# Kernel tuning notes

Measured on AMD Instinct MI355X. Metric: run time of the kernel, lower is better.

The kernel has to match this reference:

```python
import jax, jax.numpy as jnp
import numpy as np

A = 9          # num anchors (RPN.anchor_list)
H = W = 32     # feature-map spatial size (scaled-up from 7x7)
HID = 256      # ProposalModule hidden dim
THRESH = 0.5       # inference() thresh default
NMS_THRESH = 0.7   # inference() nms_thresh default
N = H * W * A


def _conv(x, w, b):
    y = jax.lax.conv_general_dilated(x, w, (1, 1), 'SAME',
                                     dimension_numbers=('NCHW', 'OIHW', 'NCHW'))
    return y + b[None, :, None, None]


def _pairwise_iou(boxes):
    # boxes: (N,4) [x1,y1,x2,y2]
    x1, y1, x2, y2 = boxes[:, 0], boxes[:, 1], boxes[:, 2], boxes[:, 3]
    area = jnp.maximum(x2 - x1, 0.) * jnp.maximum(y2 - y1, 0.)
    iw = jnp.maximum(jnp.minimum(x2[:, None], x2[None, :]) - jnp.maximum(x1[:, None], x1[None, :]), 0.)
    ih = jnp.maximum(jnp.minimum(y2[:, None], y2[None, :]) - jnp.maximum(y1[:, None], y1[None, :]), 0.)
    inter = iw * ih
    return inter / (area[:, None] + area[None, :] - inter + 1e-8)


def _nms_keep(boxes, scores, valid, iou_thresh):
    # greedy NMS over ALL boxes; invalid (below conf-thresh) boxes start suppressed
    n = boxes.shape[0]
    order = jnp.argsort(-scores)
    b = boxes[order]
    v = valid[order]
    iou = _pairwise_iou(b)            # (N,N) -- dominant memory traffic
    idx = jnp.arange(n)

    def body(i, sup):
        alive = jnp.logical_not(sup[i])
        return sup | (alive & (iou[i] > iou_thresh) & (idx > i))

    sup = jax.lax.fori_loop(0, n, body, jnp.logical_not(v))
    return jnp.zeros(n, bool).at[order].set(jnp.logical_not(sup))


def setup_inputs() -> dict:
    key = jax.random.key(0)
    ks = jax.random.split(key, 4)
    feat = jax.random.normal(ks[0], (1, 1280, H, W), jnp.float32)
    anchors_wh = jnp.array([[1, 1], [2, 2], [3, 3], [4, 4], [5, 5],
                            [2, 3], [3, 2], [3, 5], [5, 3]], jnp.float32)
    w1 = jax.random.normal(ks[1], (HID, 1280, 3, 3), jnp.float32) * 0.01
    b1 = jnp.zeros((HID,), jnp.float32)
    w2 = jax.random.normal(ks[2], (6 * A, HID, 1, 1), jnp.float32) * 0.05
    b2 = jax.random.normal(ks[3], (6 * A,), jnp.float32) * 0.05
    return {"feat": feat, "anchors_wh": anchors_wh, "w1": w1, "b1": b1, "w2": w2, "b2": b2}


def reference(feat, anchors_wh, w1, b1, w2, b2):
    # ProposalModule: 3x3 conv + LeakyReLU + 1x1 conv to 6A channels (dropout is identity at inference)
    h = jax.nn.leaky_relu(_conv(feat, w1, b1), 0.01)
    out = _conv(h, w2, b2)[0].reshape(A, 6, H, W)   # batch 1 -> (A,6,H,W)
    conf = jax.nn.sigmoid(out[:, 0])                 # (A,H,W), sigmoid(conf_scores[:,0])
    offs = out[:, 2:6].transpose(0, 2, 3, 1)         # (A,H,W,4) = offsets.permute(0,2,3,1)

    # GenerateGrid: cell centers at +0.5; GenerateAnchor: wh-sized boxes on each center
    xs = jnp.arange(W, dtype=feat.dtype) + 0.5
    ys = jnp.arange(H, dtype=feat.dtype) + 0.5
    cx = xs[None, None, :]
    cy = ys[None, :, None]
    aw = anchors_wh[:, 0][:, None, None]
    ah = anchors_wh[:, 1][:, None, None]

    tx, ty, tw, th = offs[..., 0], offs[..., 1], offs[..., 2], offs[..., 3]
    pcx = cx + tx * aw
    pcy = cy + ty * ah
    pw = aw * jnp.exp(tw)
    ph = ah * jnp.exp(th)
    boxes = jnp.stack([pcx - pw / 2, pcy - ph / 2, pcx + pw / 2, pcy + ph / 2], -1)  # (A,H,W,4)

    conf_f = conf.transpose(1, 2, 0).reshape(-1)          # (H*W*A,) = permute(1,2,0).reshape(-1)
    boxes_f = boxes.transpose(1, 2, 0, 3).reshape(-1, 4)  # (H*W*A,4)

    valid = conf_f > THRESH
    scores = jnp.where(valid, conf_f, -1.0)
    keep = _nms_keep(boxes_f, scores, valid, NMS_THRESH)

    k = keep.astype(boxes_f.dtype)[:, None]
    # fixed-shape masked output: kept rows are [x1,y1,x2,y2,conf], suppressed rows are 0
    return jnp.concatenate([boxes_f * k, conf_f[:, None] * k], axis=-1)  # (N,5)
```

## Files before the change

kernel.cpp:

```cpp
#include <hip/hip_runtime.h>
#include <math.h>

#define NPIX 1024
#define NBOX 9216
#define ECAP 6144

typedef unsigned long long u64;

#define O_PART     0u
#define O_H        0u
#define O_BOXES    1048576u
#define O_CONF     1196032u
#define O_KEYS     1232896u
#define O_ORDER    1306624u
#define O_SBOX     1343488u
#define O_SAREA    1490944u
#define O_EDGES    1527808u
#define O_KEEPW    1552384u
#define O_RPART    1553920u
#define O_VCNT     16777216u
#define O_ECNT     16777220u


__global__ __launch_bounds__(256, 4) void conv1_kernel(const float* __restrict__ feat,
                                                       const float* __restrict__ w1,
                                                       float* __restrict__ partial,
                                                       int* __restrict__ VE) {
    const int kc  = blockIdx.x;
    const int cog = blockIdx.y;
    const int tid = threadIdx.x;
    const int x0 = (tid & 7) * 4;
    const int y  = tid >> 3;
    const int ci0 = kc * 80;
    const int co0 = cog * 4;

    if (kc == 0 && cog == 0 && tid < 2) VE[tid] = 0;

    __shared__ float sf[8 * 34 * 32];

    for (int e = tid; e < 8 * 2 * 32; e += 256) {
        int ci_l = e >> 6, r = (e >> 5) & 1, c = e & 31;
        sf[(ci_l * 34 + r * 33) * 32 + c] = 0.f;
    }

    float acc[4][4];
#pragma unroll
    for (int a = 0; a < 4; ++a)
#pragma unroll
        for (int b = 0; b < 4; ++b) acc[a][b] = 0.f;

    const float* wbase = w1 + (size_t)co0 * 11520 + (size_t)ci0 * 9;

    for (int chunk = 0; chunk < 10; ++chunk) {
        const int cbase = ci0 + chunk * 8;
        __syncthreads();
        {
            const float4* fg = (const float4*)(feat + (size_t)cbase * NPIX);
#pragma unroll
            for (int k = 0; k < 8; ++k) {
                int e = tid + k * 256;
                int ci_l = e >> 8, rem = e & 255;
                int row = rem >> 3, f4c = rem & 7;
                float4 v = fg[ci_l * 256 + rem];
                *(float4*)&sf[(ci_l * 34 + row + 1) * 32 + f4c * 4] = v;
            }
        }
        __syncthreads();

#pragma unroll
        for (int cil = 0; cil < 8; ++cil) {
            float f[3][6];
            const float* base = &sf[(cil * 34 + y) * 32];
#pragma unroll
            for (int dy = 0; dy < 3; ++dy) {
                const float* rp = base + dy * 32;
                float4 mid = *(const float4*)(rp + x0);
                float lft = __int_as_float(__builtin_amdgcn_update_dpp(
                    0, __float_as_int(mid.w), 0x111 , 0xF, 0xF, true));
                float rgt = __int_as_float(__builtin_amdgcn_update_dpp(
                    0, __float_as_int(mid.x), 0x101 , 0xF, 0xF, true));
                f[dy][0] = (x0 == 0) ? 0.f : lft;
                f[dy][1] = mid.x; f[dy][2] = mid.y; f[dy][3] = mid.z; f[dy][4] = mid.w;
                f[dy][5] = (x0 == 28) ? 0.f : rgt;
            }
#pragma unroll
            for (int co = 0; co < 4; ++co) {
                const float* wrow = wbase + (size_t)co * 11520 +
                                    (size_t)(chunk * 8 + cil) * 9;
                float wv[9];
#pragma unroll
                for (int t = 0; t < 9; ++t) wv[t] = wrow[t];
#pragma unroll
                for (int dy = 0; dy < 3; ++dy)
#pragma unroll
                    for (int dx = 0; dx < 3; ++dx) {
                        float wgt = wv[dy * 3 + dx];
#pragma unroll
                        for (int px = 0; px < 4; ++px)
                            acc[co][px] = fmaf(f[dy][px + dx], wgt, acc[co][px]);
                    }
            }
        }
    }

    const int pix = y * 32 + x0;
#pragma unroll
    for (int co = 0; co < 4; ++co) {
        float4 v = {acc[co][0], acc[co][1], acc[co][2], acc[co][3]};
        *(float4*)&partial[((size_t)kc * 256 + co0 + co) * NPIX + pix] = v;
    }
}

__global__ __launch_bounds__(256) void conv1_reduce(float* part_h,
                                                    const float* __restrict__ b1) {
    int i = blockIdx.x * 256 + threadIdx.x;
    float s = b1[i >> 10];
#pragma unroll
    for (int kc = 0; kc < 16; ++kc) s += part_h[(size_t)kc * 262144 + i];
    part_h[i] = s > 0.f ? s : 0.01f * s;
}

__global__ __launch_bounds__(256) void conv2_decode(const float* __restrict__ h,
                                                    const float* __restrict__ w2,
                                                    const float* __restrict__ b2,
                                                    const float* __restrict__ anchors,
                                                    float* __restrict__ boxes,
                                                    float* __restrict__ conf_arr,
                                                    u64* __restrict__ keys,
                                                    int* __restrict__ Vcnt) {
    int gid = blockIdx.x * 256 + threadIdx.x;
    int box = gid >> 3, q = gid & 7;
    int a = box >> 10, p = box & 1023;
    const float* hq  = h + (size_t)(q * 32) * NPIX + p;
    const float* wq  = w2 + (size_t)(a * 6) * 256 + q * 32;
    float s0 = 0.f, s2 = 0.f, s3 = 0.f, s4 = 0.f, s5 = 0.f;
#pragma unroll 4
    for (int ci = 0; ci < 32; ++ci) {
        float hv = hq[(size_t)ci * NPIX];
        s0 = fmaf(hv, wq[0 * 256 + ci], s0);
        s2 = fmaf(hv, wq[2 * 256 + ci], s2);
        s3 = fmaf(hv, wq[3 * 256 + ci], s3);
        s4 = fmaf(hv, wq[4 * 256 + ci], s4);
        s5 = fmaf(hv, wq[5 * 256 + ci], s5);
    }
    s0 += __shfl_xor(s0, 1); s0 += __shfl_xor(s0, 2); s0 += __shfl_xor(s0, 4);
    s2 += __shfl_xor(s2, 1); s2 += __shfl_xor(s2, 2); s2 += __shfl_xor(s2, 4);
    s3 += __shfl_xor(s3, 1); s3 += __shfl_xor(s3, 2); s3 += __shfl_xor(s3, 4);
    s4 += __shfl_xor(s4, 1); s4 += __shfl_xor(s4, 2); s4 += __shfl_xor(s4, 4);
    s5 += __shfl_xor(s5, 1); s5 += __shfl_xor(s5, 2); s5 += __shfl_xor(s5, 4);
    if (q == 0) {
        s0 += b2[a * 6 + 0];
        s2 += b2[a * 6 + 2];
        s3 += b2[a * 6 + 3];
        s4 += b2[a * 6 + 4];
        s5 += b2[a * 6 + 5];
        float conf = 1.f / (1.f + expf(-s0));
        float x = (float)(p & 31), yy = (float)(p >> 5);
        float cx = x + 0.5f, cy = yy + 0.5f;
        float aw = anchors[a * 2 + 0], ah = anchors[a * 2 + 1];
        float pcx = cx + s2 * aw, pcy = cy + s3 * ah;
        float pw = aw * expf(s4), ph = ah * expf(s5);
        int idx = p * 9 + a;
        boxes[idx * 4 + 0] = pcx - pw / 2.f;
        boxes[idx * 4 + 1] = pcy - ph / 2.f;
        boxes[idx * 4 + 2] = pcx + pw / 2.f;
        boxes[idx * 4 + 3] = pcy + ph / 2.f;
        conf_arr[idx] = conf;
        bool valid = conf > 0.5f;
        float score = valid ? conf : -1.0f;
        unsigned int sb = __float_as_uint(score);
        sb = (sb & 0x80000000u) ? ~sb : (sb | 0x80000000u);
        keys[idx] = ((u64)sb << 32) | (unsigned int)(~idx);
        if (valid) atomicAdd(Vcnt, 1);
    }
}

__global__ __launch_bounds__(256) void rank_partial(const u64* __restrict__ keys,
                                                    int* __restrict__ rpart) {
    __shared__ u64 sk[256];
    int i = blockIdx.x * 256 + threadIdx.x;
    sk[threadIdx.x] = keys[blockIdx.y * 256 + threadIdx.x];
    __syncthreads();
    u64 ki = keys[i];
    int c = 0;
#pragma unroll 8
    for (int j = 0; j < 256; ++j) c += (sk[j] > ki) ? 1 : 0;
    rpart[blockIdx.y * NBOX + i] = c;
}

__global__ __launch_bounds__(256) void rank_reduce_gather(const int* __restrict__ rpart,
                                                          const float* __restrict__ boxes,
                                                          int* __restrict__ order,
                                                          float* __restrict__ sbox,
                                                          float* __restrict__ sarea) {
    int i = blockIdx.x * 256 + threadIdx.x;
    int r = 0;
    for (int b = 0; b < 36; ++b) r += rpart[b * NBOX + i];
    order[r] = i;
    float x1 = boxes[i * 4 + 0], y1 = boxes[i * 4 + 1];
    float x2 = boxes[i * 4 + 2], y2 = boxes[i * 4 + 3];
    sbox[r * 4 + 0] = x1; sbox[r * 4 + 1] = y1;
    sbox[r * 4 + 2] = x2; sbox[r * 4 + 3] = y2;
    sarea[r] = fmaxf(x2 - x1, 0.f) * fmaxf(y2 - y1, 0.f);
}

__global__ __launch_bounds__(256) void nms_edges(const float* __restrict__ sbox,
                                                 const float* __restrict__ sarea,
                                                 const int* __restrict__ Vp,
                                                 unsigned* __restrict__ edges,
                                                 int* __restrict__ Ecnt) {
    int V = *Vp;
    int lane = threadIdx.x & 63;
    for (int i = blockIdx.x; i < V; i += 2048) {
        float x1i = sbox[i * 4 + 0], y1i = sbox[i * 4 + 1];
        float x2i = sbox[i * 4 + 2], y2i = sbox[i * 4 + 3];
        float ai = sarea[i];
        for (int j = i + 1 + threadIdx.x; ; j += 256) {
            bool active = (j < V);
            if (__ballot(active) == 0ull) break;
            bool hit = false;
            if (active) {
                float x1j = sbox[j * 4 + 0], y1j = sbox[j * 4 + 1];
                float x2j = sbox[j * 4 + 2], y2j = sbox[j * 4 + 3];
                float iw = fmaxf(fminf(x2i, x2j) - fmaxf(x1i, x1j), 0.f);
                float ih = fmaxf(fminf(y2i, y2j) - fmaxf(y1i, y1j), 0.f);
                float inter = iw * ih;
                float iou = inter / (ai + sarea[j] - inter + 1e-8f);
                hit = iou > 0.7f;
            }
            u64 bal = __ballot(hit);
            if (bal) {
                int cnt = __popcll(bal);
                unsigned base = 0;
                if (lane == 0) base = (unsigned)atomicAdd(Ecnt, cnt);
                base = (unsigned)__shfl((int)base, 0, 64);
                if (hit) {
                    int pos = (int)base + __popcll(bal & ((1ull << lane) - 1ull));
                    if (pos < ECAP) edges[pos] = ((unsigned)j << 16) | (unsigned)i;
                }
            }
        }
    }
}

__global__ __launch_bounds__(256) void nms_resolve(const unsigned* __restrict__ edges,
                                                   const int* __restrict__ Ep,
                                                   const int* __restrict__ Vp,
                                                   u64* __restrict__ keepw) {
    __shared__ unsigned se[ECAP];
    __shared__ unsigned ss[ECAP];
    __shared__ u64 sup[144];
    const int tid = threadIdx.x;
    int E = *Ep; if (E > ECAP) E = ECAP;
    const int V = *Vp;
    for (int e = tid; e < E; e += 256) se[e] = edges[e];
    for (int w = tid; w < 144; w += 256) sup[w] = 0;
    __syncthreads();
    for (int e = tid; e < E; e += 256) {
        unsigned k = se[e];
        int r = 0;
        for (int q = 0; q < E; ++q) r += (se[q] < k) ? 1 : 0;
        ss[r] = k;
    }
    __syncthreads();
    if (tid == 0) {
        for (int e = 0; e < E; ++e) {
            unsigned k = ss[e];
            int i = (int)(k & 0xffffu), j = (int)(k >> 16);
            if (!((sup[i >> 6] >> (i & 63)) & 1ull))
                sup[j >> 6] |= 1ull << (j & 63);
        }
    }
    __syncthreads();
    for (int w = tid; w < 144; w += 256) {
        int base = w * 64;
        u64 vm;
        if (base + 64 <= V) vm = ~0ull;
        else if (base >= V) vm = 0ull;
        else vm = (1ull << (V - base)) - 1ull;
        keepw[w] = ~sup[w] & vm;
    }
}

__global__ __launch_bounds__(256) void finalize(const int* __restrict__ order,
                                                const int* __restrict__ Vp,
                                                const u64* __restrict__ keepw,
                                                const float* __restrict__ boxes,
                                                const float* __restrict__ conf_arr,
                                                float* __restrict__ out) {
    int p = blockIdx.x * 256 + threadIdx.x;
    int V = *Vp;
    int o = order[p];
    bool keep = false;
    if (p < V) keep = (keepw[p >> 6] >> (p & 63)) & 1ull;
    float k = keep ? 1.f : 0.f;
    out[o * 5 + 0] = boxes[o * 4 + 0] * k;
    out[o * 5 + 1] = boxes[o * 4 + 1] * k;
    out[o * 5 + 2] = boxes[o * 4 + 2] * k;
    out[o * 5 + 3] = boxes[o * 4 + 3] * k;
    out[o * 5 + 4] = conf_arr[o] * k;
}

extern "C" void kernel_launch(void* const* d_in, const int* in_sizes, int n_in,
                              void* d_out, int out_size, void* d_ws, size_t ws_size,
                              hipStream_t stream) {
    const float* feat    = (const float*)d_in[0];
    const float* anchors = (const float*)d_in[1];
    const float* w1      = (const float*)d_in[2];
    const float* b1      = (const float*)d_in[3];
    const float* w2      = (const float*)d_in[4];
    const float* b2      = (const float*)d_in[5];
    float* out = (float*)d_out;

    char* ws = (char*)d_ws;
    float* partial = (float*)(ws + O_PART);
    float* h       = (float*)(ws + O_H);
    float* boxes   = (float*)(ws + O_BOXES);
    float* conf    = (float*)(ws + O_CONF);
    u64*   keys    = (u64*)(ws + O_KEYS);
    int* rpart     = (int*)(ws + O_RPART);
    int* order     = (int*)(ws + O_ORDER);
    float* sbox    = (float*)(ws + O_SBOX);
    float* sarea   = (float*)(ws + O_SAREA);
    int* Vcnt      = (int*)(ws + O_VCNT);
    int* Ecnt      = (int*)(ws + O_ECNT);
    u64* keepw     = (u64*)(ws + O_KEEPW);
    unsigned* edges = (unsigned*)(ws + O_EDGES);

    conv1_kernel<<<dim3(16, 64), 256, 0, stream>>>(feat, w1, partial, Vcnt);
    conv1_reduce<<<1024, 256, 0, stream>>>(partial, b1);
    conv2_decode<<<288, 256, 0, stream>>>(h, w2, b2, anchors, boxes, conf, keys, Vcnt);
    rank_partial<<<dim3(36, 36), 256, 0, stream>>>(keys, rpart);
    rank_reduce_gather<<<36, 256, 0, stream>>>(rpart, boxes, order, sbox, sarea);
    nms_edges<<<2048, 256, 0, stream>>>(sbox, sarea, Vcnt, edges, Ecnt);
    nms_resolve<<<1, 256, 0, stream>>>(edges, Ecnt, Vcnt, keepw);
    finalize<<<36, 256, 0, stream>>>(order, Vcnt, keepw, boxes, conf, out);
}
```

Baseline: 226.1 us.

## Fuse post-conv pipeline stages into one cooperative persistent kernel with grid syncs

Replaces the seven kernels after conv1 (reduce, conv2/decode, rank, gather, NMS edges, resolve, finalize) with a single cooperative kernel of 512 blocks separated by grid.sync barriers. It falls back to the original launch sequence if the cooperative launch fails. The aim is to remove per-kernel launch gaps and tail effects in the small latency-bound stages. In exchange, each stage runs on a fixed 512-block grid instead of its own launch shape, the big shared arrays limit occupancy, and grid-wide barriers have their own cost.

```diff
diff --git a/kernel.cpp b/kernel.cpp
--- a/kernel.cpp
+++ b/kernel.cpp
@@ -1,9 +1,13 @@
 #include <hip/hip_runtime.h>
+#include <hip/hip_cooperative_groups.h>
 #include <math.h>
+
+namespace cg = cooperative_groups;
 
 #define NPIX 1024
 #define NBOX 9216
 #define ECAP 6144
+#define TGRID 512
 
 typedef unsigned long long u64;
 
@@ -301,6 +305,202 @@
     out[o * 5 + 4] = conf_arr[o] * k;
 }
 
+__global__ __launch_bounds__(256, 2) void tail_mega(float* part_h,
+                                                    const float* __restrict__ b1,
+                                                    const float* __restrict__ w2,
+                                                    const float* __restrict__ b2,
+                                                    const float* __restrict__ anchors,
+                                                    float* __restrict__ boxes,
+                                                    float* __restrict__ conf_arr,
+                                                    u64* __restrict__ keys,
+                                                    int* __restrict__ Vcnt,
+                                                    int* __restrict__ Ecnt,
+                                                    int* __restrict__ rpart,
+                                                    int* __restrict__ order,
+                                                    float* __restrict__ sbox,
+                                                    float* __restrict__ sarea,
+                                                    unsigned* __restrict__ edges,
+                                                    u64* __restrict__ keepw,
+                                                    float* __restrict__ out) {
+    cg::grid_group grid = cg::this_grid();
+    const int tid = threadIdx.x;
+    const int bid = blockIdx.x;
+
+    __shared__ u64 sk[256];
+    __shared__ unsigned se[ECAP];
+    __shared__ unsigned ss[ECAP];
+    __shared__ u64 sup[144];
+
+    for (int i = bid * 256 + tid; i < 262144; i += TGRID * 256) {
+        float s = b1[i >> 10];
+#pragma unroll
+        for (int kc = 0; kc < 16; ++kc) s += part_h[(size_t)kc * 262144 + i];
+        part_h[i] = s > 0.f ? s : 0.01f * s;
+    }
+    grid.sync();
+
+    for (int vb = bid; vb < 288; vb += TGRID) {
+        int gid = vb * 256 + tid;
+        int box = gid >> 3, q = gid & 7;
+        int a = box >> 10, p = box & 1023;
+        const float* hq  = part_h + (size_t)(q * 32) * NPIX + p;
+        const float* wq  = w2 + (size_t)(a * 6) * 256 + q * 32;
+        float s0 = 0.f, s2 = 0.f, s3 = 0.f, s4 = 0.f, s5 = 0.f;
+#pragma unroll 4
+        for (int ci = 0; ci < 32; ++ci) {
+            float hv = hq[(size_t)ci * NPIX];
+            s0 = fmaf(hv, wq[0 * 256 + ci], s0);
+            s2 = fmaf(hv, wq[2 * 256 + ci], s2);
+            s3 = fmaf(hv, wq[3 * 256 + ci], s3);
+            s4 = fmaf(hv, wq[4 * 256 + ci], s4);
+            s5 = fmaf(hv, wq[5 * 256 + ci], s5);
+        }
+        s0 += __shfl_xor(s0, 1); s0 += __shfl_xor(s0, 2); s0 += __shfl_xor(s0, 4);
+        s2 += __shfl_xor(s2, 1); s2 += __shfl_xor(s2, 2); s2 += __shfl_xor(s2, 4);
+        s3 += __shfl_xor(s3, 1); s3 += __shfl_xor(s3, 2); s3 += __shfl_xor(s3, 4);
+        s4 += __shfl_xor(s4, 1); s4 += __shfl_xor(s4, 2); s4 += __shfl_xor(s4, 4);
+        s5 += __shfl_xor(s5, 1); s5 += __shfl_xor(s5, 2); s5 += __shfl_xor(s5, 4);
+        if (q == 0) {
+            s0 += b2[a * 6 + 0];
+            s2 += b2[a * 6 + 2];
+            s3 += b2[a * 6 + 3];
+            s4 += b2[a * 6 + 4];
+            s5 += b2[a * 6 + 5];
+            float conf = 1.f / (1.f + expf(-s0));
+            float x = (float)(p & 31), yy = (float)(p >> 5);
+            float cx = x + 0.5f, cy = yy + 0.5f;
+            float aw = anchors[a * 2 + 0], ah = anchors[a * 2 + 1];
+            float pcx = cx + s2 * aw, pcy = cy + s3 * ah;
+            float pw = aw * expf(s4), ph = ah * expf(s5);
+            int idx = p * 9 + a;
+            boxes[idx * 4 + 0] = pcx - pw / 2.f;
+            boxes[idx * 4 + 1] = pcy - ph / 2.f;
+            boxes[idx * 4 + 2] = pcx + pw / 2.f;
+            boxes[idx * 4 + 3] = pcy + ph / 2.f;
+            conf_arr[idx] = conf;
+            bool valid = conf > 0.5f;
+            float score = valid ? conf : -1.0f;
+            unsigned int sb = __float_as_uint(score);
+            sb = (sb & 0x80000000u) ? ~sb : (sb | 0x80000000u);
+            keys[idx] = ((u64)sb << 32) | (unsigned int)(~idx);
+            if (valid) atomicAdd(Vcnt, 1);
+        }
+    }
+    grid.sync();
+
+    for (int v = bid; v < 1296; v += TGRID) {
+        int bx = v % 36, by = v / 36;
+        sk[tid] = keys[by * 256 + tid];
+        __syncthreads();
+        int i = bx * 256 + tid;
+        u64 ki = keys[i];
+        int c = 0;
+#pragma unroll 8
+        for (int j = 0; j < 256; ++j) c += (sk[j] > ki) ? 1 : 0;
+        rpart[by * NBOX + i] = c;
+        __syncthreads();
+    }
+    grid.sync();
+
+    for (int v = bid; v < 36; v += TGRID) {
+        int i = v * 256 + tid;
+        int r = 0;
+        for (int b = 0; b < 36; ++b) r += rpart[b * NBOX + i];
+        order[r] = i;
+        float x1 = boxes[i * 4 + 0], y1 = boxes[i * 4 + 1];
+        float x2 = boxes[i * 4 + 2], y2 = boxes[i * 4 + 3];
+        sbox[r * 4 + 0] = x1; sbox[r * 4 + 1] = y1;
+        sbox[r * 4 + 2] = x2; sbox[r * 4 + 3] = y2;
+        sarea[r] = fmaxf(x2 - x1, 0.f) * fmaxf(y2 - y1, 0.f);
+    }
+    grid.sync();
+
+    {
+        int V = *Vcnt;
+        int lane = tid & 63;
+        for (int i = bid; i < V; i += TGRID) {
+            float x1i = sbox[i * 4 + 0], y1i = sbox[i * 4 + 1];
+            float x2i = sbox[i * 4 + 2], y2i = sbox[i * 4 + 3];
+            float ai = sarea[i];
+            for (int j = i + 1 + tid; ; j += 256) {
+                bool active = (j < V);
+                if (__ballot(active) == 0ull) break;
+                bool hit = false;
+                if (active) {
+                    float x1j = sbox[j * 4 + 0], y1j = sbox[j * 4 + 1];
+                    float x2j = sbox[j * 4 + 2], y2j = sbox[j * 4 + 3];
+                    float iw = fmaxf(fminf(x2i, x2j) - fmaxf(x1i, x1j), 0.f);
+                    float ih = fmaxf(fminf(y2i, y2j) - fmaxf(y1i, y1j), 0.f);
+                    float inter = iw * ih;
+                    float iou = inter / (ai + sarea[j] - inter + 1e-8f);
+                    hit = iou > 0.7f;
+                }
+                u64 bal = __ballot(hit);
+                if (bal) {
+                    int cnt = __popcll(bal);
+                    unsigned base = 0;
+                    if (lane == 0) base = (unsigned)atomicAdd(Ecnt, cnt);
+                    base = (unsigned)__shfl((int)base, 0, 64);
+                    if (hit) {
+                        int pos = (int)base + __popcll(bal & ((1ull << lane) - 1ull));
+                        if (pos < ECAP) edges[pos] = ((unsigned)j << 16) | (unsigned)i;
+                    }
+                }
+            }
+        }
+    }
+    grid.sync();
+
+    if (bid == 0) {
+        int E = *Ecnt; if (E > ECAP) E = ECAP;
+        const int V = *Vcnt;
+        for (int e = tid; e < E; e += 256) se[e] = edges[e];
+        for (int w = tid; w < 144; w += 256) sup[w] = 0;
+        __syncthreads();
+        for (int e = tid; e < E; e += 256) {
+            unsigned k = se[e];
+            int r = 0;
+            for (int q = 0; q < E; ++q) r += (se[q] < k) ? 1 : 0;
+            ss[r] = k;
+        }
+        __syncthreads();
+        if (tid == 0) {
+            for (int e = 0; e < E; ++e) {
+                unsigned k = ss[e];
+                int i = (int)(k & 0xffffu), j = (int)(k >> 16);
+                if (!((sup[i >> 6] >> (i & 63)) & 1ull))
+                    sup[j >> 6] |= 1ull << (j & 63);
+            }
+        }
+        __syncthreads();
+        for (int w = tid; w < 144; w += 256) {
+            int base = w * 64;
+            u64 vm;
+            if (base + 64 <= V) vm = ~0ull;
+            else if (base >= V) vm = 0ull;
+            else vm = (1ull << (V - base)) - 1ull;
+            keepw[w] = ~sup[w] & vm;
+        }
+    }
+    grid.sync();
+
+    {
+        int V = *Vcnt;
+        for (int v = bid; v < 36; v += TGRID) {
+            int p = v * 256 + tid;
+            int o = order[p];
+            bool keep = false;
+            if (p < V) keep = (keepw[p >> 6] >> (p & 63)) & 1ull;
+            float k = keep ? 1.f : 0.f;
+            out[o * 5 + 0] = boxes[o * 4 + 0] * k;
+            out[o * 5 + 1] = boxes[o * 4 + 1] * k;
+            out[o * 5 + 2] = boxes[o * 4 + 2] * k;
+            out[o * 5 + 3] = boxes[o * 4 + 3] * k;
+            out[o * 5 + 4] = conf_arr[o] * k;
+        }
+    }
+}
+
 extern "C" void kernel_launch(void* const* d_in, const int* in_sizes, int n_in,
                               void* d_out, int out_size, void* d_ws, size_t ws_size,
                               hipStream_t stream) {
@@ -328,11 +528,21 @@
     unsigned* edges = (unsigned*)(ws + O_EDGES);
 
     conv1_kernel<<<dim3(16, 64), 256, 0, stream>>>(feat, w1, partial, Vcnt);
-    conv1_reduce<<<1024, 256, 0, stream>>>(partial, b1);
-    conv2_decode<<<288, 256, 0, stream>>>(h, w2, b2, anchors, boxes, conf, keys, Vcnt);
-    rank_partial<<<dim3(36, 36), 256, 0, stream>>>(keys, rpart);
-    rank_reduce_gather<<<36, 256, 0, stream>>>(rpart, boxes, order, sbox, sarea);
-    nms_edges<<<2048, 256, 0, stream>>>(sbox, sarea, Vcnt, edges, Ecnt);
-    nms_resolve<<<1, 256, 0, stream>>>(edges, Ecnt, Vcnt, keepw);
-    finalize<<<36, 256, 0, stream>>>(order, Vcnt, keepw, boxes, conf, out);
-}
+
+    void* args[] = {&partial, &b1, &w2, &b2, &anchors, &boxes, &conf, &keys,
+                    &Vcnt, &Ecnt, &rpart, &order, &sbox, &sarea, &edges,
+                    &keepw, &out};
+    hipError_t err = hipLaunchCooperativeKernel((const void*)tail_mega,
+                                                dim3(TGRID), dim3(256),
+                                                args, 0, stream);
+    if (err != hipSuccess) {
+        conv1_reduce<<<1024, 256, 0, stream>>>(partial, b1);
+        conv2_decode<<<288, 256, 0, stream>>>(h, w2, b2, anchors, boxes, conf,
+                                              keys, Vcnt);
+        rank_partial<<<dim3(36, 36), 256, 0, stream>>>(keys, rpart);
+        rank_reduce_gather<<<36, 256, 0, stream>>>(rpart, boxes, order, sbox, sarea);
+        nms_edges<<<2048, 256, 0, stream>>>(sbox, sarea, Vcnt, edges, Ecnt);
+        nms_resolve<<<1, 256, 0, stream>>>(edges, Ecnt, Vcnt, keepw);
+        finalize<<<36, 256, 0, stream>>>(order, Vcnt, keepw, boxes, conf, out);
+    }
+}
```

After: 534.0 us. +136.2%, slower.

## Resolve NMS suppression by parallel fixed-point iteration instead of sort and serial scan

Applied to the files above, without the earlier changes.

Replaces the O(E^2) rank sort of the edge list and the single-thread greedy scan with an iterative parallel relaxation. Each round, every edge (i,j) marks j as suppressed in a double-buffered bitmask if i is not suppressed in the previous round. Rounds stop once the mask no longer changes. Because edges always point from higher to lower score, this converges to the greedy NMS result. The number of rounds equals the longest suppression chain, so deep chains could require many block-wide synchronising passes.

```diff
diff --git a/kernel.cpp b/kernel.cpp
--- a/kernel.cpp
+++ b/kernel.cpp
@@ -248,37 +248,41 @@
                                                    const int* __restrict__ Vp,
                                                    u64* __restrict__ keepw) {
     __shared__ unsigned se[ECAP];
-    __shared__ unsigned ss[ECAP];
-    __shared__ u64 sup[144];
+    __shared__ u64 sup[2][144];
+    __shared__ int chg;
     const int tid = threadIdx.x;
     int E = *Ep; if (E > ECAP) E = ECAP;
     const int V = *Vp;
     for (int e = tid; e < E; e += 256) se[e] = edges[e];
-    for (int w = tid; w < 144; w += 256) sup[w] = 0;
+    for (int w = tid; w < 144; w += 256) sup[0][w] = 0;
     __syncthreads();
-    for (int e = tid; e < E; e += 256) {
-        unsigned k = se[e];
-        int r = 0;
-        for (int q = 0; q < E; ++q) r += (se[q] < k) ? 1 : 0;
-        ss[r] = k;
-    }
-    __syncthreads();
-    if (tid == 0) {
-        for (int e = 0; e < E; ++e) {
-            unsigned k = ss[e];
+    int p = 0;
+    for (int it = 0; it < E + 2; ++it) {
+        for (int w = tid; w < 144; w += 256) sup[1 - p][w] = 0;
+        if (tid == 0) chg = 0;
+        __syncthreads();
+        for (int e = tid; e < E; e += 256) {
+            unsigned k = se[e];
             int i = (int)(k & 0xffffu), j = (int)(k >> 16);
-            if (!((sup[i >> 6] >> (i & 63)) & 1ull))
-                sup[j >> 6] |= 1ull << (j & 63);
+            if (!((sup[p][i >> 6] >> (i & 63)) & 1ull))
+                atomicOr(&sup[1 - p][j >> 6], 1ull << (j & 63));
         }
-    }
-    __syncthreads();
+        __syncthreads();
+        for (int w = tid; w < 144; w += 256)
+            if (sup[1 - p][w] != sup[p][w]) chg = 1;
+        __syncthreads();
+        int done = !chg;
+        __syncthreads();
+        p ^= 1;
+        if (done) break;
+    }
     for (int w = tid; w < 144; w += 256) {
         int base = w * 64;
         u64 vm;
         if (base + 64 <= V) vm = ~0ull;
         else if (base >= V) vm = 0ull;
         else vm = (1ull << (V - base)) - 1ull;
-        keepw[w] = ~sup[w] & vm;
+        keepw[w] = ~sup[p][w] & vm;
     }
 }
 
```

New measurement: 203.7 us, median of 3. 1.11x faster.
